# Kernel optimization log

Measured on AMD Instinct MI355X. Metric: run time of the kernel, lower is better.

## Reference

```python
import jax, jax.numpy as jnp
import numpy as np

SEQ_LEN = 8192
HIDDEN = 4096

def setup_inputs() -> dict:
    key = jax.random.key(0)
    k1, k2 = jax.random.split(key)
    hidden = jax.random.normal(k1, (HIDDEN,), dtype=jnp.float32)
    encoder_outputs = jax.random.normal(k2, (SEQ_LEN, 1, HIDDEN), dtype=jnp.float32)
    return {"hidden": hidden, "encoder_outputs": encoder_outputs}

def reference(hidden, encoder_outputs):
    # encoder_outputs: [S, 1, H] -> [S, H]
    enc = encoder_outputs.squeeze(1)
    # energies[i] = dot(hidden, enc[i])  (one batched GEMV instead of a per-step loop)
    energies = enc @ hidden  # [S]
    attn = jax.nn.softmax(energies, axis=0)  # [S]
    # output = enc^T @ attn  (torch.mm(enc.T, attn.unsqueeze(1)).squeeze(1))
    output = enc.T @ attn  # [H]
    return output, attn[:, None]
```

## Files before the change

### kernel.cpp

```cpp
#include <hip/hip_runtime.h>
#include <math.h>

#define S_LEN 8192
#define HDIM  4096
#define H4    (HDIM / 4)
#define P1_BLOCK 512
#define P1_WAVES (P1_BLOCK / 64)
#define FB_ATTN 8

__device__ __forceinline__ float wave_reduce_sum(float x) {
#pragma unroll
  for (int o = 32; o > 0; o >>= 1) x += __shfl_xor(x, o, 64);
  return x;
}
__device__ __forceinline__ float wave_reduce_max(float x) {
#pragma unroll
  for (int o = 32; o > 0; o >>= 1) x = fmaxf(x, __shfl_xor(x, o, 64));
  return x;
}

__global__ __launch_bounds__(P1_BLOCK) void pass1_k(
    const float* __restrict__ enc, const float* __restrict__ hidden,
    float* __restrict__ energies, float* __restrict__ mb, float* __restrict__ lb,
    float* __restrict__ opart, int rpb) {
  const int t = threadIdx.x;
  const int b = blockIdx.x;
  const int row0 = b * rpb;
  const int row1 = min(S_LEN, row0 + rpb);

  const float4* hv = (const float4*)hidden;
  const float4 h0 = hv[t];
  const float4 h1 = hv[t + P1_BLOCK];

  float4 a0 = {0.f, 0.f, 0.f, 0.f};
  float4 a1 = {0.f, 0.f, 0.f, 0.f};
  float m = -INFINITY, l = 0.f;

  __shared__ float red[P1_WAVES];
  const int wid = t >> 6;
  const bool lane0 = (t & 63) == 0;

  const float4* encv = (const float4*)enc;
  for (int r = row0; r < row1; ++r) {
    const float4* rp = encv + (size_t)r * H4;
    const float4 v0 = rp[t];
    const float4 v1 = rp[t + P1_BLOCK];
    float d = v0.x * h0.x + v0.y * h0.y + v0.z * h0.z + v0.w * h0.w
            + v1.x * h1.x + v1.y * h1.y + v1.z * h1.z + v1.w * h1.w;
    d = wave_reduce_sum(d);
    if (lane0) red[wid] = d;
    __syncthreads();
    float e = 0.f;
#pragma unroll
    for (int i = 0; i < P1_WAVES; ++i) e += red[i];
    __syncthreads();
    if (t == 0) energies[r] = e;

    const float mn = fmaxf(m, e);
    const float sc = __expf(m - mn);
    const float w  = __expf(e - mn);
    l = l * sc + w;
    a0.x = fmaf(a0.x, sc, w * v0.x);
    a0.y = fmaf(a0.y, sc, w * v0.y);
    a0.z = fmaf(a0.z, sc, w * v0.z);
    a0.w = fmaf(a0.w, sc, w * v0.w);
    a1.x = fmaf(a1.x, sc, w * v1.x);
    a1.y = fmaf(a1.y, sc, w * v1.y);
    a1.z = fmaf(a1.z, sc, w * v1.z);
    a1.w = fmaf(a1.w, sc, w * v1.w);
    m = mn;
  }

  float4* op = (float4*)(opart + (size_t)b * HDIM);
  op[t] = a0;
  op[t + P1_BLOCK] = a1;
  if (t == 0) { mb[b] = m; lb[b] = l; }
}

__global__ __launch_bounds__(1024) void stats_k(
    const float* __restrict__ mb, const float* __restrict__ lb,
    float* __restrict__ stats, int Gu) {
  const int t = threadIdx.x;
  __shared__ float red[16];
  float mv = (t < Gu) ? mb[t] : -INFINITY;
  float mw = wave_reduce_max(mv);
  if ((t & 63) == 0) red[t >> 6] = mw;
  __syncthreads();
  float gm = -INFINITY;
#pragma unroll
  for (int i = 0; i < 16; ++i) gm = fmaxf(gm, red[i]);
  __syncthreads();
  float li = (t < Gu) ? lb[t] * __expf(mb[t] - gm) : 0.f;
  float lw = wave_reduce_sum(li);
  if ((t & 63) == 0) red[t >> 6] = lw;
  __syncthreads();
  float L = 0.f;
#pragma unroll
  for (int i = 0; i < 16; ++i) L += red[i];
  if (t == 0) { stats[0] = gm; stats[1] = L; stats[2] = 1.f / L; }
}

__global__ __launch_bounds__(256) void finalize_k(
    const float* __restrict__ opart, const float* __restrict__ mb,
    const float* __restrict__ energies, const float* __restrict__ stats,
    float* __restrict__ out, int Gu, int Bout, int gpb) {
  const int t = threadIdx.x;
  const float gm  = stats[0];
  const float invL = stats[2];
  if ((int)blockIdx.x < Bout) {
    const int g0 = blockIdx.x * gpb;
    const int g1 = min(Gu, g0 + gpb);
    float4 acc[4] = {{0,0,0,0},{0,0,0,0},{0,0,0,0},{0,0,0,0}};
    for (int g = g0; g < g1; ++g) {
      const float w = __expf(mb[g] - gm) * invL;
      const float4* op = (const float4*)(opart + (size_t)g * HDIM);
#pragma unroll
      for (int k = 0; k < 4; ++k) {
        const float4 v = op[t + k * 256];
        acc[k].x += w * v.x; acc[k].y += w * v.y;
        acc[k].z += w * v.z; acc[k].w += w * v.w;
      }
    }
#pragma unroll
    for (int k = 0; k < 4; ++k) {
      const int h = (t + k * 256) * 4;
      atomicAdd(&out[h + 0], acc[k].x);
      atomicAdd(&out[h + 1], acc[k].y);
      atomicAdd(&out[h + 2], acc[k].z);
      atomicAdd(&out[h + 3], acc[k].w);
    }
  } else {
    const int i4 = ((int)blockIdx.x - Bout) * 256 + t;
    const float4 e = ((const float4*)energies)[i4];
    float4 a;
    a.x = __expf(e.x - gm) * invL;
    a.y = __expf(e.y - gm) * invL;
    a.z = __expf(e.z - gm) * invL;
    a.w = __expf(e.w - gm) * invL;
    ((float4*)(out + HDIM))[i4] = a;
  }
}

extern "C" void kernel_launch(void* const* d_in, const int* in_sizes, int n_in,
                              void* d_out, int out_size, void* d_ws, size_t ws_size,
                              hipStream_t stream) {
  const float* hidden = (const float*)d_in[0];
  const float* enc    = (const float*)d_in[1];
  float* out = (float*)d_out;
  float* wsf = (float*)d_ws;

  float* energies = wsf;
  float* mb       = wsf + 8192;
  float* lb       = wsf + 9216;
  float* stats    = wsf + 10240;
  float* opart    = wsf + 10256;

  const size_t avail_f = ws_size / 4;
  int Gmax = (avail_f > 10256) ? (int)((avail_f - 10256) / HDIM) : 1;
  int G = Gmax < 512 ? Gmax : 512;
  if (G < 1) G = 1;
  const int rpb = (S_LEN + G - 1) / G;
  const int Gu  = (S_LEN + rpb - 1) / rpb;

  hipMemsetAsync(d_out, 0, HDIM * sizeof(float), stream);
  pass1_k<<<Gu, P1_BLOCK, 0, stream>>>(enc, hidden, energies, mb, lb, opart, rpb);
  stats_k<<<1, 1024, 0, stream>>>(mb, lb, stats, Gu);

  int Bout = Gu < 128 ? Gu : 128;
  const int gpb = (Gu + Bout - 1) / Bout;
  Bout = (Gu + gpb - 1) / gpb;
  finalize_k<<<Bout + FB_ATTN, 256, 0, stream>>>(opart, mb, energies, stats, out, Gu, Bout, gpb);
}
```

Before: 216.2 us.

## Batch four rows per iteration in pass1 and fold stats kernel into finalize

The first pass now loads four encoder rows per iteration, reduces their four dot products together, and pays for two block barriers per four rows instead of per row. The online-softmax rescale is applied once per batch. The separate single-block stats kernel is removed, and every finalize block now recomputes the global max and normalizer from the per-block partials, which saves one launch at the cost of redundant small reductions. Register pressure in pass1 goes up with four rows of float4 data held live.

```diff
diff --git a/kernel.cpp b/kernel.cpp
--- a/kernel.cpp
+++ b/kernel.cpp
@@ -5,7 +5,8 @@
 #define HDIM  4096
 #define H4    (HDIM / 4)
 #define P1_BLOCK 512
-#define P1_WAVES (P1_BLOCK / 64)
+#define P1_WAVES 8
+#define RB 4
 #define FB_ATTN 8
 
 __device__ __forceinline__ float wave_reduce_sum(float x) {
@@ -17,6 +18,18 @@
 #pragma unroll
   for (int o = 32; o > 0; o >>= 1) x = fmaxf(x, __shfl_xor(x, o, 64));
   return x;
+}
+__device__ __forceinline__ float dot4(float4 a, float4 b) {
+  return a.x * b.x + a.y * b.y + a.z * b.z + a.w * b.w;
+}
+__device__ __forceinline__ float upd(float a, float sc, const float* w,
+                                     float x0, float x1, float x2, float x3) {
+  float r = a * sc;
+  r = fmaf(w[0], x0, r);
+  r = fmaf(w[1], x1, r);
+  r = fmaf(w[2], x2, r);
+  r = fmaf(w[3], x3, r);
+  return r;
 }
 
 __global__ __launch_bounds__(P1_BLOCK) void pass1_k(
@@ -36,38 +49,67 @@
   float4 a1 = {0.f, 0.f, 0.f, 0.f};
   float m = -INFINITY, l = 0.f;
 
-  __shared__ float red[P1_WAVES];
+  __shared__ float red[RB * P1_WAVES];
   const int wid = t >> 6;
   const bool lane0 = (t & 63) == 0;
-
   const float4* encv = (const float4*)enc;
-  for (int r = row0; r < row1; ++r) {
-    const float4* rp = encv + (size_t)r * H4;
-    const float4 v0 = rp[t];
-    const float4 v1 = rp[t + P1_BLOCK];
-    float d = v0.x * h0.x + v0.y * h0.y + v0.z * h0.z + v0.w * h0.w
-            + v1.x * h1.x + v1.y * h1.y + v1.z * h1.z + v1.w * h1.w;
-    d = wave_reduce_sum(d);
-    if (lane0) red[wid] = d;
+
+  for (int r0 = row0; r0 < row1; r0 += RB) {
+    const int nr = min(RB, row1 - r0);
+    float4 v[RB][2];
+    float d[RB];
+#pragma unroll
+    for (int r = 0; r < RB; ++r) {
+      if (r < nr) {
+        const float4* rp = encv + (size_t)(r0 + r) * H4;
+        v[r][0] = rp[t];
+        v[r][1] = rp[t + P1_BLOCK];
+      } else {
+        v[r][0] = make_float4(0.f, 0.f, 0.f, 0.f);
+        v[r][1] = make_float4(0.f, 0.f, 0.f, 0.f);
+      }
+    }
+#pragma unroll
+    for (int r = 0; r < RB; ++r)
+      d[r] = dot4(v[r][0], h0) + dot4(v[r][1], h1);
+#pragma unroll
+    for (int o = 32; o > 0; o >>= 1) {
+#pragma unroll
+      for (int r = 0; r < RB; ++r) d[r] += __shfl_xor(d[r], o, 64);
+    }
+    if (lane0) {
+#pragma unroll
+      for (int r = 0; r < RB; ++r) red[r * P1_WAVES + wid] = d[r];
+    }
     __syncthreads();
-    float e = 0.f;
-#pragma unroll
-    for (int i = 0; i < P1_WAVES; ++i) e += red[i];
+    float e[RB];
+#pragma unroll
+    for (int r = 0; r < RB; ++r) {
+      const float4 q0 = *(const float4*)&red[r * P1_WAVES];
+      const float4 q1 = *(const float4*)&red[r * P1_WAVES + 4];
+      e[r] = (q0.x + q0.y + q0.z + q0.w) + (q1.x + q1.y + q1.z + q1.w);
+    }
     __syncthreads();
-    if (t == 0) energies[r] = e;
-
-    const float mn = fmaxf(m, e);
+    if (t == 0) {
+      for (int r = 0; r < nr; ++r) energies[r0 + r] = e[r];
+    }
+    float mn = m;
+#pragma unroll
+    for (int r = 0; r < RB; ++r)
+      if (r < nr) mn = fmaxf(mn, e[r]);
     const float sc = __expf(m - mn);
-    const float w  = __expf(e - mn);
-    l = l * sc + w;
-    a0.x = fmaf(a0.x, sc, w * v0.x);
-    a0.y = fmaf(a0.y, sc, w * v0.y);
-    a0.z = fmaf(a0.z, sc, w * v0.z);
-    a0.w = fmaf(a0.w, sc, w * v0.w);
-    a1.x = fmaf(a1.x, sc, w * v1.x);
-    a1.y = fmaf(a1.y, sc, w * v1.y);
-    a1.z = fmaf(a1.z, sc, w * v1.z);
-    a1.w = fmaf(a1.w, sc, w * v1.w);
+    float w[RB];
+#pragma unroll
+    for (int r = 0; r < RB; ++r) w[r] = (r < nr) ? __expf(e[r] - mn) : 0.f;
+    l = l * sc + w[0] + w[1] + w[2] + w[3];
+    a0.x = upd(a0.x, sc, w, v[0][0].x, v[1][0].x, v[2][0].x, v[3][0].x);
+    a0.y = upd(a0.y, sc, w, v[0][0].y, v[1][0].y, v[2][0].y, v[3][0].y);
+    a0.z = upd(a0.z, sc, w, v[0][0].z, v[1][0].z, v[2][0].z, v[3][0].z);
+    a0.w = upd(a0.w, sc, w, v[0][0].w, v[1][0].w, v[2][0].w, v[3][0].w);
+    a1.x = upd(a1.x, sc, w, v[0][1].x, v[1][1].x, v[2][1].x, v[3][1].x);
+    a1.y = upd(a1.y, sc, w, v[0][1].y, v[1][1].y, v[2][1].y, v[3][1].y);
+    a1.z = upd(a1.z, sc, w, v[0][1].z, v[1][1].z, v[2][1].z, v[3][1].z);
+    a1.w = upd(a1.w, sc, w, v[0][1].w, v[1][1].w, v[2][1].w, v[3][1].w);
     m = mn;
   }
 
@@ -77,36 +119,29 @@
   if (t == 0) { mb[b] = m; lb[b] = l; }
 }
 
-__global__ __launch_bounds__(1024) void stats_k(
-    const float* __restrict__ mb, const float* __restrict__ lb,
-    float* __restrict__ stats, int Gu) {
-  const int t = threadIdx.x;
-  __shared__ float red[16];
-  float mv = (t < Gu) ? mb[t] : -INFINITY;
-  float mw = wave_reduce_max(mv);
-  if ((t & 63) == 0) red[t >> 6] = mw;
-  __syncthreads();
-  float gm = -INFINITY;
-#pragma unroll
-  for (int i = 0; i < 16; ++i) gm = fmaxf(gm, red[i]);
-  __syncthreads();
-  float li = (t < Gu) ? lb[t] * __expf(mb[t] - gm) : 0.f;
-  float lw = wave_reduce_sum(li);
-  if ((t & 63) == 0) red[t >> 6] = lw;
-  __syncthreads();
-  float L = 0.f;
-#pragma unroll
-  for (int i = 0; i < 16; ++i) L += red[i];
-  if (t == 0) { stats[0] = gm; stats[1] = L; stats[2] = 1.f / L; }
-}
-
 __global__ __launch_bounds__(256) void finalize_k(
     const float* __restrict__ opart, const float* __restrict__ mb,
-    const float* __restrict__ energies, const float* __restrict__ stats,
+    const float* __restrict__ lb, const float* __restrict__ energies,
     float* __restrict__ out, int Gu, int Bout, int gpb) {
   const int t = threadIdx.x;
-  const float gm  = stats[0];
-  const float invL = stats[2];
+  const int wid = t >> 6;
+  const bool lane0 = (t & 63) == 0;
+  __shared__ float smax[4], ssum[4];
+
+  float mv = -INFINITY;
+  for (int g = t; g < Gu; g += 256) mv = fmaxf(mv, mb[g]);
+  mv = wave_reduce_max(mv);
+  if (lane0) smax[wid] = mv;
+  __syncthreads();
+  const float gm = fmaxf(fmaxf(smax[0], smax[1]), fmaxf(smax[2], smax[3]));
+
+  float lv = 0.f;
+  for (int g = t; g < Gu; g += 256) lv += lb[g] * __expf(mb[g] - gm);
+  lv = wave_reduce_sum(lv);
+  if (lane0) ssum[wid] = lv;
+  __syncthreads();
+  const float invL = 1.f / (ssum[0] + ssum[1] + ssum[2] + ssum[3]);
+
   if ((int)blockIdx.x < Bout) {
     const int g0 = blockIdx.x * gpb;
     const int g1 = min(Gu, g0 + gpb);
@@ -117,8 +152,10 @@
 #pragma unroll
       for (int k = 0; k < 4; ++k) {
         const float4 v = op[t + k * 256];
-        acc[k].x += w * v.x; acc[k].y += w * v.y;
-        acc[k].z += w * v.z; acc[k].w += w * v.w;
+        acc[k].x = fmaf(w, v.x, acc[k].x);
+        acc[k].y = fmaf(w, v.y, acc[k].y);
+        acc[k].z = fmaf(w, v.z, acc[k].z);
+        acc[k].w = fmaf(w, v.w, acc[k].w);
       }
     }
 #pragma unroll
@@ -152,11 +189,10 @@
   float* energies = wsf;
   float* mb       = wsf + 8192;
   float* lb       = wsf + 9216;
-  float* stats    = wsf + 10240;
-  float* opart    = wsf + 10256;
+  float* opart    = wsf + 10240;
 
   const size_t avail_f = ws_size / 4;
-  int Gmax = (avail_f > 10256) ? (int)((avail_f - 10256) / HDIM) : 1;
+  int Gmax = (avail_f > 10240) ? (int)((avail_f - 10240) / HDIM) : 1;
   int G = Gmax < 512 ? Gmax : 512;
   if (G < 1) G = 1;
   const int rpb = (S_LEN + G - 1) / G;
@@ -164,10 +200,9 @@
 
   hipMemsetAsync(d_out, 0, HDIM * sizeof(float), stream);
   pass1_k<<<Gu, P1_BLOCK, 0, stream>>>(enc, hidden, energies, mb, lb, opart, rpb);
-  stats_k<<<1, 1024, 0, stream>>>(mb, lb, stats, Gu);
 
   int Bout = Gu < 128 ? Gu : 128;
   const int gpb = (Gu + Bout - 1) / Bout;
   Bout = (Gu + gpb - 1) / gpb;
-  finalize_k<<<Bout + FB_ATTN, 256, 0, stream>>>(opart, mb, energies, stats, out, Gu, Bout, gpb);
-}
+  finalize_k<<<Bout + FB_ATTN, 256, 0, stream>>>(opart, mb, lb, energies, out, Gu, Bout, gpb);
+}
```

Result: faster. 210.9 us (-2.4%).
